# Kernel optimization log

Hardware: AMD Instinct MI355X
Metric: run time of the kernel (lower is better)

The kernel has to match this reference:

```python
import jax, jax.numpy as jnp
import numpy as np

H_WIN, W_WIN = 5, 5
PADH, PADW = H_WIN // 2, W_WIN // 2
SIGMA = 1.0
GAUSS_DEN = 2.0 * SIGMA ** 2
NCLASSES = 20


def setup_inputs() -> dict:
    key = jax.random.key(0)
    k1, k2, k3 = jax.random.split(key, 3)
    xyz = jax.random.normal(k1, (2, 3, 64, 2048), dtype=jnp.float32)
    softmax = jax.random.uniform(k2, (2, 20, 64, 2048), dtype=jnp.float32)
    mask = jax.random.randint(k3, (2, 64, 2048), 0, 2, dtype=jnp.int32)
    return {"xyz": xyz, "softmax": softmax, "mask": mask}


def _window_indices(H, W):
    # rows: zero-padded in height (like F.unfold padding), cols: circular in width
    dh = jnp.arange(-PADH, PADH + 1)
    rows = jnp.arange(H)[:, None] + dh              # (H, h)
    valid = (rows >= 0) & (rows < H)                # (H, h)
    rows_c = jnp.clip(rows, 0, H - 1)
    dw = jnp.arange(-PADW, PADW + 1)
    cols = (jnp.arange(W)[:, None] + dw) % W        # (W, w) circular
    return rows_c, valid, cols


def _gather_windows(a, rows_c, valid, cols):
    # a: (..., H, W) -> (..., H, h, W, w); out-of-range rows -> 0 (zero padding)
    g = a[..., rows_c, :]                           # (..., H, h, W)
    g = jnp.where(valid[:, :, None], g, jnp.zeros((), a.dtype))
    return g[..., cols]                             # (..., H, h, W, w)


def reference(xyz, softmax, mask):
    N, C, H, W = softmax.shape
    sm = softmax * mask.astype(softmax.dtype)[:, None]   # mask invalid pixels
    rows_c, valid, cols = _window_indices(H, W)

    x, y, z = xyz[:, 0], xyz[:, 1], xyz[:, 2]            # each (N, H, W)
    wx = _gather_windows(x, rows_c, valid, cols)         # (N, H, h, W, w)
    wy = _gather_windows(y, rows_c, valid, cols)
    wz = _gather_windows(z, rows_c, valid, cols)
    cx = x[:, :, None, :, None]
    cy = y[:, :, None, :, None]
    cz = z[:, :, None, :, None]
    dist2 = (wx - cx) ** 2 + (wy - cy) ** 2 + (wz - cz) ** 2
    gauss = jnp.exp(-dist2 / GAUSS_DEN)                  # (N, H, h, W, w)

    sm_w = _gather_windows(sm, rows_c, valid, cols)      # (N, C, H, h, W, w)
    out = (sm_w * gauss[:, None]).sum(axis=(3, 5))       # (N, C, H, W)
    return out
```

## Files before the change

kernel.cpp:

```cpp
#include <hip/hip_runtime.h>

constexpr int N = 2;
constexpr int C = 20;
constexpr int H = 64;
constexpr int W = 2048;
constexpr int HW = H * W;

constexpr int TILE  = 256;
constexpr int LCOLS = TILE + 8;
constexpr int F4    = LCOLS / 4;
constexpr int ITEMS = 5 * F4;

__global__ __launch_bounds__(256)
void lcl_xyz_kernel(const float* __restrict__ xyz,
                    const float* __restrict__ softmax,
                    const int* __restrict__ mask,
                    float* __restrict__ out) {
    __shared__ float sx[5][LCOLS];
    __shared__ float sy[5][LCOLS];
    __shared__ float sz[5][LCOLS];
    __shared__ int   sk[5][LCOLS];
    __shared__ float sp[5][LCOLS];

    const int t  = threadIdx.x;
    const int bw = blockIdx.x & 7;
    const int h  = (blockIdx.x >> 3) & 63;
    const int n  = blockIdx.x >> 9;
    const int w0 = bw * TILE;

    const float* xb = xyz + (size_t)(n * 3 + 0) * HW;
    const float* yb = xyz + (size_t)(n * 3 + 1) * HW;
    const float* zb = xyz + (size_t)(n * 3 + 2) * HW;
    const int*   mb = mask + (size_t)n * HW;

    for (int it = t; it < ITEMS; it += 256) {
        int r  = it / F4;
        int k  = it - r * F4;
        int hc = min(max(h - 2 + r, 0), H - 1);
        int col = (w0 - 4 + 4 * k) & (W - 1);
        int rowoff = hc * W + col;
        *(float4*)&sx[r][4 * k] = *(const float4*)(xb + rowoff);
        *(float4*)&sy[r][4 * k] = *(const float4*)(yb + rowoff);
        *(float4*)&sz[r][4 * k] = *(const float4*)(zb + rowoff);
        *(int4*)  &sk[r][4 * k] = *(const int4*)  (mb + rowoff);
    }
    __syncthreads();

    const int ci = t + 4;
    const float cx = sx[2][ci];
    const float cy = sy[2][ci];
    const float cz = sz[2][ci];

    float wgt[25];
    #pragma unroll
    for (int r = 0; r < 5; ++r) {
        bool valid = (unsigned)(h - 2 + r) < (unsigned)H;
        #pragma unroll
        for (int j = 0; j < 5; ++j) {
            int cc = t + 2 + j;
            float dx = sx[r][cc] - cx;
            float dy = sy[r][cc] - cy;
            float dz = sz[r][cc] - cz;
            float d2 = dx * dx + dy * dy + dz * dz;
            float g  = __expf(-0.5f * d2);
            g = (valid && sk[r][cc]) ? g : 0.0f;
            wgt[r * 5 + j] = g;
        }
    }

    const float* smb = softmax + (size_t)n * C * HW;
    float*       op  = out + (size_t)n * C * HW + (size_t)h * W + w0 + t;

    for (int c = 0; c < C; ++c) {
        __syncthreads();
        const float* sc = smb + (size_t)c * HW;
        for (int it = t; it < ITEMS; it += 256) {
            int r  = it / F4;
            int k  = it - r * F4;
            int hc = min(max(h - 2 + r, 0), H - 1);
            int col = (w0 - 4 + 4 * k) & (W - 1);
            *(float4*)&sp[r][4 * k] = *(const float4*)(sc + hc * W + col);
        }
        __syncthreads();

        float acc = 0.0f;
        #pragma unroll
        for (int r = 0; r < 5; ++r) {
            #pragma unroll
            for (int j = 0; j < 5; ++j) {
                acc = fmaf(wgt[r * 5 + j], sp[r][t + 2 + j], acc);
            }
        }
        op[(size_t)c * HW] = acc;
    }
}

extern "C" void kernel_launch(void* const* d_in, const int* in_sizes, int n_in,
                              void* d_out, int out_size, void* d_ws, size_t ws_size,
                              hipStream_t stream) {
    const float* xyz     = (const float*)d_in[0];
    const float* softmax = (const float*)d_in[1];
    const int*   mask    = (const int*)d_in[2];
    float*       out     = (float*)d_out;

    const int grid = N * H * (W / TILE);
    lcl_xyz_kernel<<<grid, 256, 0, stream>>>(xyz, softmax, mask, out);
}
```

Baseline: 28.62 us.

## Double-buffer softmax tiles via async global-to-LDS loads, two outputs per thread

Softmax channel tiles are now double-buffered in shared memory using direct global-to-LDS loads. The next channel's tile is prefetched while the current one is being accumulated, which removes one barrier per channel. Each thread now produces two adjacent output columns with vectorized float2 LDS reads and stores, which halves the grid and amortizes the halo loads. The risks are lower occupancy from the doubled LDS buffer and fewer blocks, and a reliance on the barrier to wait for the async LDS loads to complete.

```diff
diff --git a/kernel.cpp b/kernel.cpp
--- a/kernel.cpp
+++ b/kernel.cpp
@@ -6,12 +6,19 @@
 constexpr int W = 2048;
 constexpr int HW = H * W;
 
-constexpr int TILE  = 256;
+constexpr int BLK   = 256;
+constexpr int OPT   = 2;
+constexpr int TILE  = BLK * OPT;
 constexpr int LCOLS = TILE + 8;
 constexpr int F4    = LCOLS / 4;
 constexpr int ITEMS = 5 * F4;
 
-__global__ __launch_bounds__(256)
+#define GLDS16(g, l)                                                        \
+    __builtin_amdgcn_global_load_lds(                                       \
+        (const __attribute__((address_space(1))) void*)(g),                 \
+        (__attribute__((address_space(3))) void*)(l), 16, 0, 0)
+
+__global__ __launch_bounds__(BLK)
 void lcl_xyz_kernel(const float* __restrict__ xyz,
                     const float* __restrict__ softmax,
                     const int* __restrict__ mask,
@@ -20,78 +27,123 @@
     __shared__ float sy[5][LCOLS];
     __shared__ float sz[5][LCOLS];
     __shared__ int   sk[5][LCOLS];
-    __shared__ float sp[5][LCOLS];
+    __shared__ float sp[2][5][LCOLS];
 
     const int t  = threadIdx.x;
-    const int bw = blockIdx.x & 7;
-    const int h  = (blockIdx.x >> 3) & 63;
-    const int n  = blockIdx.x >> 9;
+    const int bw = blockIdx.x & 3;
+    const int h  = (blockIdx.x >> 2) & 63;
+    const int n  = blockIdx.x >> 8;
     const int w0 = bw * TILE;
 
-    const float* xb = xyz + (size_t)(n * 3 + 0) * HW;
-    const float* yb = xyz + (size_t)(n * 3 + 1) * HW;
-    const float* zb = xyz + (size_t)(n * 3 + 2) * HW;
-    const int*   mb = mask + (size_t)n * HW;
+    int hc[5];
+    #pragma unroll
+    for (int r = 0; r < 5; ++r) hc[r] = min(max(h - 2 + r, 0), H - 1);
 
-    for (int it = t; it < ITEMS; it += 256) {
-        int r  = it / F4;
-        int k  = it - r * F4;
-        int hc = min(max(h - 2 + r, 0), H - 1);
-        int col = (w0 - 4 + 4 * k) & (W - 1);
-        int rowoff = hc * W + col;
-        *(float4*)&sx[r][4 * k] = *(const float4*)(xb + rowoff);
-        *(float4*)&sy[r][4 * k] = *(const float4*)(yb + rowoff);
-        *(float4*)&sz[r][4 * k] = *(const float4*)(zb + rowoff);
-        *(int4*)  &sk[r][4 * k] = *(const int4*)  (mb + rowoff);
+    const float* xb  = xyz + (size_t)(n * 3 + 0) * HW;
+    const float* yb  = xyz + (size_t)(n * 3 + 1) * HW;
+    const float* zb  = xyz + (size_t)(n * 3 + 2) * HW;
+    const int*   mb  = mask + (size_t)n * HW;
+    const float* smb = softmax + (size_t)n * C * HW;
+
+    #pragma unroll
+    for (int s = 0; s < 3; ++s) {
+        int it = t + BLK * s;
+        if (it < ITEMS) {
+            int r   = it / F4;
+            int k   = it - r * F4;
+            int off = hc[r] * W + ((w0 - 4 + 4 * k) & (W - 1));
+            GLDS16(xb + off, (char*)&sx[0][0] + it * 16);
+            GLDS16(yb + off, (char*)&sy[0][0] + it * 16);
+            GLDS16(zb + off, (char*)&sz[0][0] + it * 16);
+            GLDS16(mb + off, (char*)&sk[0][0] + it * 16);
+        }
+    }
+    #pragma unroll
+    for (int s = 0; s < 3; ++s) {
+        int it = t + BLK * s;
+        if (it < ITEMS) {
+            int r   = it / F4;
+            int k   = it - r * F4;
+            int off = hc[r] * W + ((w0 - 4 + 4 * k) & (W - 1));
+            GLDS16(smb + off, (char*)&sp[0][0][0] + it * 16);
+        }
     }
     __syncthreads();
 
-    const int ci = t + 4;
-    const float cx = sx[2][ci];
-    const float cy = sy[2][ci];
-    const float cz = sz[2][ci];
+    const int base = 2 * t + 2;
+    const float cx0 = sx[2][base + 2], cx1 = sx[2][base + 3];
+    const float cy0 = sy[2][base + 2], cy1 = sy[2][base + 3];
+    const float cz0 = sz[2][base + 2], cz1 = sz[2][base + 3];
 
-    float wgt[25];
+    float wa[5][5], wb[5][5];
     #pragma unroll
     for (int r = 0; r < 5; ++r) {
-        bool valid = (unsigned)(h - 2 + r) < (unsigned)H;
+        const bool hv = (unsigned)(h - 2 + r) < (unsigned)H;
+        float xv[6], yv[6], zv[6];
+        int   mv[6];
+        *(float2*)&xv[0] = *(const float2*)&sx[r][base];
+        *(float2*)&xv[2] = *(const float2*)&sx[r][base + 2];
+        *(float2*)&xv[4] = *(const float2*)&sx[r][base + 4];
+        *(float2*)&yv[0] = *(const float2*)&sy[r][base];
+        *(float2*)&yv[2] = *(const float2*)&sy[r][base + 2];
+        *(float2*)&yv[4] = *(const float2*)&sy[r][base + 4];
+        *(float2*)&zv[0] = *(const float2*)&sz[r][base];
+        *(float2*)&zv[2] = *(const float2*)&sz[r][base + 2];
+        *(float2*)&zv[4] = *(const float2*)&sz[r][base + 4];
+        *(int2*)&mv[0]   = *(const int2*)&sk[r][base];
+        *(int2*)&mv[2]   = *(const int2*)&sk[r][base + 2];
+        *(int2*)&mv[4]   = *(const int2*)&sk[r][base + 4];
         #pragma unroll
         for (int j = 0; j < 5; ++j) {
-            int cc = t + 2 + j;
-            float dx = sx[r][cc] - cx;
-            float dy = sy[r][cc] - cy;
-            float dz = sz[r][cc] - cz;
-            float d2 = dx * dx + dy * dy + dz * dz;
-            float g  = __expf(-0.5f * d2);
-            g = (valid && sk[r][cc]) ? g : 0.0f;
-            wgt[r * 5 + j] = g;
+            {
+                float dx = xv[j] - cx0, dy = yv[j] - cy0, dz = zv[j] - cz0;
+                float g  = __expf(-0.5f * (dx * dx + dy * dy + dz * dz));
+                wa[r][j] = (hv && mv[j]) ? g : 0.0f;
+            }
+            {
+                float dx = xv[j + 1] - cx1, dy = yv[j + 1] - cy1, dz = zv[j + 1] - cz1;
+                float g  = __expf(-0.5f * (dx * dx + dy * dy + dz * dz));
+                wb[r][j] = (hv && mv[j + 1]) ? g : 0.0f;
+            }
         }
     }
 
-    const float* smb = softmax + (size_t)n * C * HW;
-    float*       op  = out + (size_t)n * C * HW + (size_t)h * W + w0 + t;
+    float* ob = out + (size_t)n * C * HW + (size_t)h * W + w0 + 2 * t;
 
     for (int c = 0; c < C; ++c) {
-        __syncthreads();
-        const float* sc = smb + (size_t)c * HW;
-        for (int it = t; it < ITEMS; it += 256) {
-            int r  = it / F4;
-            int k  = it - r * F4;
-            int hc = min(max(h - 2 + r, 0), H - 1);
-            int col = (w0 - 4 + 4 * k) & (W - 1);
-            *(float4*)&sp[r][4 * k] = *(const float4*)(sc + hc * W + col);
+        if (c + 1 < C) {
+            const float* sc = smb + (size_t)(c + 1) * HW;
+            char*        lb = (char*)&sp[(c + 1) & 1][0][0];
+            #pragma unroll
+            for (int s = 0; s < 3; ++s) {
+                int it = t + BLK * s;
+                if (it < ITEMS) {
+                    int r   = it / F4;
+                    int k   = it - r * F4;
+                    int off = hc[r] * W + ((w0 - 4 + 4 * k) & (W - 1));
+                    GLDS16(sc + off, lb + it * 16);
+                }
+            }
         }
-        __syncthreads();
 
-        float acc = 0.0f;
+        const float (*spc)[LCOLS] = sp[c & 1];
+        float a0 = 0.0f, a1 = 0.0f;
         #pragma unroll
         for (int r = 0; r < 5; ++r) {
+            float v[6];
+            *(float2*)&v[0] = *(const float2*)&spc[r][base];
+            *(float2*)&v[2] = *(const float2*)&spc[r][base + 2];
+            *(float2*)&v[4] = *(const float2*)&spc[r][base + 4];
             #pragma unroll
             for (int j = 0; j < 5; ++j) {
-                acc = fmaf(wgt[r * 5 + j], sp[r][t + 2 + j], acc);
+                a0 = fmaf(wa[r][j], v[j],     a0);
+                a1 = fmaf(wb[r][j], v[j + 1], a1);
             }
         }
-        op[(size_t)c * HW] = acc;
+        float2 o; o.x = a0; o.y = a1;
+        *(float2*)(ob + (size_t)c * HW) = o;
+
+        __syncthreads();
     }
 }
 
@@ -104,5 +156,5 @@
     float*       out     = (float*)d_out;
 
     const int grid = N * H * (W / TILE);
-    lcl_xyz_kernel<<<grid, 256, 0, stream>>>(xyz, softmax, mask, out);
+    lcl_xyz_kernel<<<grid, BLK, 0, stream>>>(xyz, softmax, mask, out);
 }
```

New measurement: 27.54 us. -3.8%, faster.
